# Performance work log

Measured on AMD Instinct MI355X. Metric: run time of the kernel, lower is better.

The kernel has to match this reference:

```python
import jax, jax.numpy as jnp
import numpy as np
import math

B, S, HID = 2, 1024, 2048
N_HEAD, N_KV = 16, 4
HEAD = HID // N_HEAD          # 128
N_REP = N_HEAD // N_KV        # 4


def setup_inputs() -> dict:
    key = jax.random.key(0)
    ks = jax.random.split(key, 5)
    x = jax.random.normal(ks[0], (B, S, HID), dtype=jnp.float32)
    # realistic RoPE tables: freqs over half dim, duplicated (rotate_half convention)
    inv_freq = 1.0 / (10000.0 ** (np.arange(0, HEAD, 2, dtype=np.float32) / HEAD))
    t = np.arange(S, dtype=np.float32)
    freqs = np.outer(t, inv_freq)                    # [S, HEAD/2]
    emb = np.concatenate([freqs, freqs], axis=-1)    # [S, HEAD]
    cos = jnp.asarray(np.cos(emb), dtype=jnp.float32)
    sin = jnp.asarray(np.sin(emb), dtype=jnp.float32)
    sc = 0.02
    wq = jax.random.normal(ks[1], (HID, HID), dtype=jnp.float32) * sc
    wk = jax.random.normal(ks[2], (HID, N_KV * HEAD), dtype=jnp.float32) * sc
    wv = jax.random.normal(ks[3], (HID, N_KV * HEAD), dtype=jnp.float32) * sc
    wo = jax.random.normal(ks[4], (HID, HID), dtype=jnp.float32) * sc
    return {"x": x, "cos": cos, "sin": sin, "wq": wq, "wk": wk, "wv": wv, "wo": wo}


def _rotate_half(t):
    h = t.shape[-1] // 2
    return jnp.concatenate([-t[..., h:], t[..., :h]], axis=-1)


def reference(x, cos, sin, wq, wk, wv, wo):
    b, s, _ = x.shape
    q = (x @ wq).reshape(b, s, N_HEAD, HEAD)   # [B,S,H,D]
    k = (x @ wk).reshape(b, s, N_KV, HEAD)     # [B,S,Kv,D]
    v = (x @ wv).reshape(b, s, N_KV, HEAD)
    # RoPE: cos/sin [S,D] -> [S,1,D], broadcasts over batch and heads
    c = cos[:s, None, :]
    sn = sin[:s, None, :]
    q = q * c + _rotate_half(q) * sn
    k = k * c + _rotate_half(k) * sn
    # GQA: repeat kv heads to match query heads
    k = jnp.repeat(k, N_REP, axis=2)           # [B,S,H,D]
    v = jnp.repeat(v, N_REP, axis=2)
    q = q.transpose(0, 2, 1, 3)                # [B,H,S,D]
    k = k.transpose(0, 2, 1, 3)
    v = v.transpose(0, 2, 1, 3)
    scores = jnp.einsum("bhqd,bhkd->bhqk", q, k) / math.sqrt(HEAD)
    causal = jnp.triu(jnp.full((s, s), -jnp.inf, dtype=scores.dtype), k=1)
    scores = scores + causal[None, None, :, :]
    probs = jax.nn.softmax(scores.astype(jnp.float32), axis=-1).astype(q.dtype)
    out = jnp.einsum("bhqk,bhkd->bhqd", probs, v)   # [B,H,S,D]
    out = out.transpose(0, 2, 1, 3).reshape(b, s, N_HEAD * HEAD)
    return out @ wo
```

## Files before the change

### kernel.cpp

```cpp
#include <hip/hip_runtime.h>
#include <hip/hip_bf16.h>
#include <math.h>
#include <stdint.h>

#define BATCH 2
#define SEQ   1024
#define HID   2048
#define NH    16
#define NKV   4
#define HEAD  128
#define MROWS (BATCH*SEQ)
#define QSC   0.08838834764831845f

typedef _Float16 f16;
typedef _Float16 f16x8 __attribute__((ext_vector_type(8)));
typedef __fp16   h16x2 __attribute__((ext_vector_type(2)));
typedef float    f32x4 __attribute__((ext_vector_type(4)));

__device__ __forceinline__ void glds16(const void* g, void* l) {
    __builtin_amdgcn_global_load_lds(
        (const __attribute__((address_space(1))) void*)g,
        (__attribute__((address_space(3))) void*)l, 16, 0, 0);
}

__device__ __forceinline__ f32x4 mfma16(f16x8 a, f16x8 b, f32x4 c) {
    return __builtin_amdgcn_mfma_f32_16x16x32_f16(a, b, c, 0, 0, 0);
}

__global__ __launch_bounds__(256)
void cvt_f32_f16(const float* __restrict__ in, f16* __restrict__ out) {
    int i = blockIdx.x * 256 + threadIdx.x;
    float4 v = ((const float4*)in)[i];
    union { ushort4 u; f16 h[4]; } o;
    o.h[0] = (f16)v.x; o.h[1] = (f16)v.y; o.h[2] = (f16)v.z; o.h[3] = (f16)v.w;
    ((ushort4*)out)[i] = o.u;
}

__global__ __launch_bounds__(256)
void transW(const float* __restrict__ w0, const float* __restrict__ w1,
            const float* __restrict__ w2, f16* __restrict__ out,
            int c1, int c2, int ld0, int ld1, int ld2) {
    __shared__ float t[64][65];
    const int n0 = blockIdx.x * 64, k0 = blockIdx.y * 64;
    const float* W; int ld, cb;
    if (n0 < c1)      { W = w0; ld = ld0; cb = 0;  }
    else if (n0 < c2) { W = w1; ld = ld1; cb = c1; }
    else              { W = w2; ld = ld2; cb = c2; }
    const int tr = threadIdx.x >> 4, tc = threadIdx.x & 15;
    #pragma unroll
    for (int i = 0; i < 4; ++i) {
        int row = tr * 4 + i;
        float4 v = *(const float4*)&W[(size_t)(k0 + row) * ld + (n0 - cb) + tc * 4];
        t[row][tc*4+0] = v.x; t[row][tc*4+1] = v.y;
        t[row][tc*4+2] = v.z; t[row][tc*4+3] = v.w;
    }
    __syncthreads();
    #pragma unroll
    for (int i = 0; i < 4; ++i) {
        int nrow = tr * 4 + i;
        union { ushort4 u; f16 h[4]; } o;
        o.h[0] = (f16)t[tc*4+0][nrow]; o.h[1] = (f16)t[tc*4+1][nrow];
        o.h[2] = (f16)t[tc*4+2][nrow]; o.h[3] = (f16)t[tc*4+3][nrow];
        *(ushort4*)&out[(size_t)(n0 + nrow) * 2048 + k0 + tc * 4] = o.u;
    }
}

template<int MODE>
__global__ __launch_bounds__(256, 2)
void gemm16(const f16* __restrict__ A, const f16* __restrict__ Bt,
            const float* __restrict__ cosp, const float* __restrict__ sinp,
            f16* __restrict__ Oq, f16* __restrict__ Ok, f16* __restrict__ Ov,
            float* __restrict__ Of)
{
    __shared__ f16 As[2][128 * 64];
    __shared__ f16 Bs[2][128 * 64];
    const int tid   = threadIdx.x;
    const int lane  = tid & 63;
    const int wid   = tid >> 6;
    const int col_l = lane & 15;
    const int hi    = lane >> 4;
    const int m0 = blockIdx.y * 128;
    const int n0 = blockIdx.x * 128;

    f32x4 acc[2][8];
    #pragma unroll
    for (int mt = 0; mt < 2; ++mt)
        #pragma unroll
        for (int nt = 0; nt < 8; ++nt)
            acc[mt][nt] = (f32x4){0.f, 0.f, 0.f, 0.f};

    auto stage = [&](int buf, int kt) {
        #pragma unroll
        for (int j = 0; j < 4; ++j) {
            int gidx = j * 256 + tid;
            int r = gidx >> 3, g = gidx & 7;
            int gs = (g ^ (r & 7)) << 3;
            glds16(A  + (size_t)(m0 + r) * 2048 + kt * 64 + gs,
                   (char*)&As[buf][0] + (size_t)(j * 256 + (wid << 6)) * 16);
            glds16(Bt + (size_t)(n0 + r) * 2048 + kt * 64 + gs,
                   (char*)&Bs[buf][0] + (size_t)(j * 256 + (wid << 6)) * 16);
        }
    };

    stage(0, 0);
    asm volatile("s_waitcnt vmcnt(0)" ::: "memory");
    __syncthreads();

    int cur = 0;
    #pragma unroll 1
    for (int kt = 0; kt < 32; ++kt) {
        if (kt < 31) stage(cur ^ 1, kt + 1);

        #pragma unroll
        for (int ks = 0; ks < 2; ++ks) {
            int gr = (ks << 2) | hi;
            int ar0 = wid * 32 + col_l;
            int ar1 = ar0 + 16;
            f16x8 a0 = *(const f16x8*)&As[cur][ar0 * 64 + ((gr ^ (ar0 & 7)) << 3)];
            f16x8 a1 = *(const f16x8*)&As[cur][ar1 * 64 + ((gr ^ (ar1 & 7)) << 3)];
            #pragma unroll
            for (int nt = 0; nt < 8; ++nt) {
                int br = nt * 16 + col_l;
                f16x8 b = *(const f16x8*)&Bs[cur][br * 64 + ((gr ^ (br & 7)) << 3)];
                acc[0][nt] = mfma16(a0, b, acc[0][nt]);
                acc[1][nt] = mfma16(a1, b, acc[1][nt]);
            }
        }

        if (kt < 31) {
            asm volatile("s_waitcnt vmcnt(0)" ::: "memory");
            __syncthreads();
            cur ^= 1;
        }
    }

    if (MODE == 0) {
        #pragma unroll
        for (int mt = 0; mt < 2; ++mt)
            #pragma unroll
            for (int r = 0; r < 4; ++r) {
                int grow = m0 + wid * 32 + mt * 16 + hi * 4 + r;
                #pragma unroll
                for (int nt = 0; nt < 8; ++nt)
                    Of[(size_t)grow * 2048 + n0 + nt * 16 + col_l] = acc[mt][nt][r];
            }
    } else if (n0 < 2048) {
        #pragma unroll
        for (int mt = 0; mt < 2; ++mt)
            #pragma unroll
            for (int r = 0; r < 4; ++r) {
                int grow = m0 + wid * 32 + mt * 16 + hi * 4 + r;
                int srow = grow & (SEQ - 1);
                #pragma unroll
                for (int nt = 0; nt < 4; ++nt) {
                    int d = nt * 16 + col_l;
                    float lo = acc[mt][nt][r], hv = acc[mt][nt + 4][r];
                    float cl = cosp[srow * HEAD + d],      sl = sinp[srow * HEAD + d];
                    float ch = cosp[srow * HEAD + d + 64], sh = sinp[srow * HEAD + d + 64];
                    Oq[(size_t)grow * 2048 + n0 + d]      = (f16)((lo * cl - hv * sl) * QSC);
                    Oq[(size_t)grow * 2048 + n0 + d + 64] = (f16)((hv * ch + lo * sh) * QSC);
                }
            }
    } else if (n0 < 2560) {
        #pragma unroll
        for (int mt = 0; mt < 2; ++mt)
            #pragma unroll
            for (int r = 0; r < 4; ++r) {
                int grow = m0 + wid * 32 + mt * 16 + hi * 4 + r;
                int srow = grow & (SEQ - 1);
                #pragma unroll
                for (int nt = 0; nt < 4; ++nt) {
                    int kc = (n0 - 2048) + nt * 16 + col_l;
                    int d  = kc & 127;
                    float lo = acc[mt][nt][r], hv = acc[mt][nt + 4][r];
                    float cl = cosp[srow * HEAD + d],      sl = sinp[srow * HEAD + d];
                    float ch = cosp[srow * HEAD + d + 64], sh = sinp[srow * HEAD + d + 64];
                    Ok[(size_t)grow * 512 + kc]      = (f16)(lo * cl - hv * sl);
                    Ok[(size_t)grow * 512 + kc + 64] = (f16)(hv * ch + lo * sh);
                }
            }
    } else {
        #pragma unroll
        for (int mt = 0; mt < 2; ++mt) {
            int grow0 = m0 + wid * 32 + mt * 16 + hi * 4;
            int bb = grow0 >> 10, s0 = grow0 & (SEQ - 1);
            #pragma unroll
            for (int nt = 0; nt < 8; ++nt) {
                int vcol = (n0 - 2560) + nt * 16 + col_l;
                int kvh = vcol >> 7, d = vcol & 127;
                union { ushort4 u; f16 h[4]; } pv;
                #pragma unroll
                for (int r = 0; r < 4; ++r) pv.h[r] = (f16)acc[mt][nt][r];
                *(ushort4*)&Ov[(size_t)((bb * 4 + kvh) * 128 + d) * 1024 + s0] = pv.u;
            }
        }
    }
}

__global__ __launch_bounds__(256, 2)
void attn16(const f16* __restrict__ q16, const f16* __restrict__ k16,
            const f16* __restrict__ vT, f16* __restrict__ attnb)
{
    __shared__ f16 Ks[2][32 * 128];
    __shared__ f16 Vs[2][128 * 32];

    const int tid   = threadIdx.x;
    const int lane  = tid & 63;
    const int wid   = tid >> 6;
    const int col_l = lane & 15;
    const int hi    = lane >> 4;

    const int bx = blockIdx.x;
    const int qt = (bx < 256) ? (15 - (bx >> 5)) : ((bx - 256) >> 5);
    const int bh = bx & 31;
    const int b  = bh >> 4;
    const int h  = bh & 15;
    const int kv = h >> 2;
    const int qrow = qt * 64 + wid * 16 + col_l;

    f16x8 qf[4];
    {
        const f16* qp = q16 + (size_t)(b * SEQ + qrow) * 2048 + h * 128 + hi * 8;
        #pragma unroll
        for (int ks = 0; ks < 4; ++ks) qf[ks] = *(const f16x8*)&qp[ks * 32];
    }
    const f16* vTg = vT + (size_t)(b * 4 + kv) * 128 * 1024;

    auto stage = [&](int buf, int kt) {
        #pragma unroll
        for (int j = 0; j < 2; ++j) {
            int gidx = j * 256 + tid;
            int r = gidx >> 4, g = gidx & 15;
            glds16(k16 + (size_t)(b * SEQ + kt * 32 + r) * 512 + kv * 128 + ((g ^ (r & 7)) << 3),
                   (char*)&Ks[buf][0] + (size_t)(j * 256 + (wid << 6)) * 16);
            int d = gidx >> 2, g2 = gidx & 3;
            glds16(vTg + (size_t)d * 1024 + kt * 32 + ((g2 ^ (d & 3)) << 3),
                   (char*)&Vs[buf][0] + (size_t)(j * 256 + (wid << 6)) * 16);
        }
    };

    f32x4 O[8];
    #pragma unroll
    for (int dt = 0; dt < 8; ++dt) O[dt] = (f32x4){0.f, 0.f, 0.f, 0.f};
    float mrun = -INFINITY, lrun = 0.f;

    const int ntiles = 2 * (qt + 1);
    stage(0, 0);
    asm volatile("s_waitcnt vmcnt(0)" ::: "memory");
    __syncthreads();

    int cur = 0;
    #pragma unroll 1
    for (int kt = 0; kt < ntiles; ++kt) {
        if (kt + 1 < ntiles) stage(cur ^ 1, kt + 1);

        f32x4 S0 = (f32x4){0.f,0.f,0.f,0.f}, S1 = (f32x4){0.f,0.f,0.f,0.f};
        #pragma unroll
        for (int ks = 0; ks < 4; ++ks) {
            int gr = (ks << 2) | hi;
            int r0 = col_l, r1 = col_l + 16;
            f16x8 kf0 = *(const f16x8*)&Ks[cur][r0 * 128 + ((gr ^ (r0 & 7)) << 3)];
            f16x8 kf1 = *(const f16x8*)&Ks[cur][r1 * 128 + ((gr ^ (r1 & 7)) << 3)];
            S0 = mfma16(kf0, qf[ks], S0);
            S1 = mfma16(kf1, qf[ks], S1);
        }
        float p[8];
        p[0]=S0[0]; p[1]=S0[1]; p[2]=S0[2]; p[3]=S0[3];
        p[4]=S1[0]; p[5]=S1[1]; p[6]=S1[2]; p[7]=S1[3];

        #pragma unroll
        for (int sl = 0; sl < 8; ++sl) {
            int kk = kt * 32 + (sl >> 2) * 16 + hi * 4 + (sl & 3);
            if (kk > qrow) p[sl] = -INFINITY;
        }

        float mt = p[0];
        #pragma unroll
        for (int sl = 1; sl < 8; ++sl) mt = fmaxf(mt, p[sl]);
        mt = fmaxf(mt, __shfl_xor(mt, 16));
        mt = fmaxf(mt, __shfl_xor(mt, 32));
        float mnew = fmaxf(mrun, mt);
        float corr = __expf(mrun - mnew);
        mrun = mnew;
        float ps = 0.f;
        #pragma unroll
        for (int sl = 0; sl < 8; ++sl) { p[sl] = __expf(p[sl] - mnew); ps += p[sl]; }
        ps += __shfl_xor(ps, 16);
        ps += __shfl_xor(ps, 32);
        lrun = lrun * corr + ps;

        union U2 { h16x2 h; int i; };
        int pk[4];
        { U2 u; u.h = __builtin_amdgcn_cvt_pkrtz(p[0], p[1]); pk[0] = u.i; }
        { U2 u; u.h = __builtin_amdgcn_cvt_pkrtz(p[2], p[3]); pk[1] = u.i; }
        { U2 u; u.h = __builtin_amdgcn_cvt_pkrtz(p[4], p[5]); pk[2] = u.i; }
        { U2 u; u.h = __builtin_amdgcn_cvt_pkrtz(p[6], p[7]); pk[3] = u.i; }
        union UA { f16x8 v; int i[4]; } ua;
        #pragma unroll
        for (int j = 0; j < 4; ++j) {
            int srcl = col_l + 16 * ((2 * hi + (j >> 1)) & 3);
            int v0 = __builtin_amdgcn_ds_bpermute(srcl << 2, pk[j & 1]);
            int v1 = __builtin_amdgcn_ds_bpermute(srcl << 2, pk[(j & 1) + 2]);
            ua.i[j] = (hi >= 2) ? v1 : v0;
        }

        float cb[4];
        #pragma unroll
        for (int r = 0; r < 4; ++r)
            cb[r] = __int_as_float(__builtin_amdgcn_ds_bpermute((hi * 4 + r) << 2,
                                                                __float_as_int(corr)));
        #pragma unroll
        for (int dt = 0; dt < 8; ++dt) {
            O[dt][0] *= cb[0]; O[dt][1] *= cb[1];
            O[dt][2] *= cb[2]; O[dt][3] *= cb[3];
        }

        #pragma unroll
        for (int dt = 0; dt < 8; ++dt) {
            int vr = dt * 16 + col_l;
            f16x8 vf = *(const f16x8*)&Vs[cur][vr * 32 + (((hi) ^ (vr & 3)) << 3)];
            O[dt] = mfma16(ua.v, vf, O[dt]);
        }

        if (kt + 1 < ntiles) {
            asm volatile("s_waitcnt vmcnt(0)" ::: "memory");
            __syncthreads();
            cur ^= 1;
        }
    }

    float linv = 1.f / lrun;
    float lb[4];
    #pragma unroll
    for (int r = 0; r < 4; ++r)
        lb[r] = __int_as_float(__builtin_amdgcn_ds_bpermute((hi * 4 + r) << 2,
                                                            __float_as_int(linv)));
    #pragma unroll
    for (int dt = 0; dt < 8; ++dt)
        #pragma unroll
        for (int r = 0; r < 4; ++r) {
            int row = b * SEQ + qt * 64 + wid * 16 + hi * 4 + r;
            attnb[(size_t)row * 2048 + h * 128 + dt * 16 + col_l] = (f16)(O[dt][r] * lb[r]);
        }
}

extern "C" void kernel_launch(void* const* d_in, const int* in_sizes, int n_in,
                              void* d_out, int out_size, void* d_ws, size_t ws_size,
                              hipStream_t stream)
{
    const float* x    = (const float*)d_in[0];
    const float* cosp = (const float*)d_in[1];
    const float* sinp = (const float*)d_in[2];
    const float* wq   = (const float*)d_in[3];
    const float* wk   = (const float*)d_in[4];
    const float* wv   = (const float*)d_in[5];
    const float* wo   = (const float*)d_in[6];
    float* out = (float*)d_out;

    char* ws = (char*)d_ws;
    f16* x16    = (f16*)(ws);
    f16* attn16v= (f16*)(ws);
    f16* Wqkvt  = (f16*)(ws + 8388608);
    f16* Wot    = (f16*)(ws + 8388608);
    f16* q16    = (f16*)(ws + 20971520);
    f16* k16    = (f16*)(ws + 29360128);
    f16* vT     = (f16*)(ws + 31457280);

    cvt_f32_f16<<<4096, 256, 0, stream>>>(x, x16);

    transW<<<dim3(48, 32), 256, 0, stream>>>(wq, wk, wv, Wqkvt, 2048, 2560, 2048, 512, 512);

    gemm16<1><<<dim3(24, 16), 256, 0, stream>>>(x16, Wqkvt, cosp, sinp,
                                                q16, k16, vT, nullptr);

    transW<<<dim3(32, 32), 256, 0, stream>>>(wo, wo, wo, Wot, 2048, 2048, 2048, 2048, 2048);

    attn16<<<dim3(512), 256, 0, stream>>>(q16, k16, vT, attn16v);

    gemm16<0><<<dim3(16, 16), 256, 0, stream>>>(attn16v, Wot, nullptr, nullptr,
                                                nullptr, nullptr, nullptr, out);
}
```

Baseline: 227.5 us.

## Shrink GEMM N-tile to 64, add XCD swizzle, move RoPE to separate kernel

The GEMM tile shrinks from 128x128 to 128x64, which doubles the grid to 768 and 512 blocks so the GPU's compute units are better filled. Block IDs are remapped across the 8 XCDs, and LDS double buffering is dropped for a single buffer with load-then-compute per k-step. The RoPE rotation and Q scaling move out of the GEMM epilogue, which can no longer see both halves of a head, into a separate elementwise kernel. This costs an extra read-write pass over Q and K, an extra f16 rounding before the rotation, and loses the overlap of loads with compute.

```diff
diff --git a/kernel.cpp b/kernel.cpp
--- a/kernel.cpp
+++ b/kernel.cpp
@@ -66,72 +66,70 @@
 }
 
 template<int MODE>
-__global__ __launch_bounds__(256, 2)
+__global__ __launch_bounds__(256)
 void gemm16(const f16* __restrict__ A, const f16* __restrict__ Bt,
-            const float* __restrict__ cosp, const float* __restrict__ sinp,
             f16* __restrict__ Oq, f16* __restrict__ Ok, f16* __restrict__ Ov,
-            float* __restrict__ Of)
+            float* __restrict__ Of, int ntn)
 {
-    __shared__ f16 As[2][128 * 64];
-    __shared__ f16 Bs[2][128 * 64];
+    __shared__ f16 As[128 * 64];
+    __shared__ f16 Bs[64 * 64];
     const int tid   = threadIdx.x;
     const int lane  = tid & 63;
     const int wid   = tid >> 6;
     const int col_l = lane & 15;
     const int hi    = lane >> 4;
-    const int m0 = blockIdx.y * 128;
-    const int n0 = blockIdx.x * 128;
-
-    f32x4 acc[2][8];
+
+    const int nwg = gridDim.x;
+    const int cpx = nwg >> 3;
+    const int bid = blockIdx.x;
+    const int sw  = (bid & 7) * cpx + (bid >> 3);
+    const int n0  = (sw % ntn) * 64;
+    const int m0  = (sw / ntn) * 128;
+
+    f32x4 acc[2][4];
     #pragma unroll
     for (int mt = 0; mt < 2; ++mt)
         #pragma unroll
-        for (int nt = 0; nt < 8; ++nt)
+        for (int nt = 0; nt < 4; ++nt)
             acc[mt][nt] = (f32x4){0.f, 0.f, 0.f, 0.f};
 
-    auto stage = [&](int buf, int kt) {
+    #pragma unroll 1
+    for (int kt = 0; kt < 32; ++kt) {
         #pragma unroll
         for (int j = 0; j < 4; ++j) {
             int gidx = j * 256 + tid;
             int r = gidx >> 3, g = gidx & 7;
             int gs = (g ^ (r & 7)) << 3;
-            glds16(A  + (size_t)(m0 + r) * 2048 + kt * 64 + gs,
-                   (char*)&As[buf][0] + (size_t)(j * 256 + (wid << 6)) * 16);
+            glds16(A + (size_t)(m0 + r) * 2048 + kt * 64 + gs,
+                   (char*)As + (size_t)(j * 256 + (wid << 6)) * 16);
+        }
+        #pragma unroll
+        for (int j = 0; j < 2; ++j) {
+            int gidx = j * 256 + tid;
+            int r = gidx >> 3, g = gidx & 7;
+            int gs = (g ^ (r & 7)) << 3;
             glds16(Bt + (size_t)(n0 + r) * 2048 + kt * 64 + gs,
-                   (char*)&Bs[buf][0] + (size_t)(j * 256 + (wid << 6)) * 16);
-        }
-    };
-
-    stage(0, 0);
-    asm volatile("s_waitcnt vmcnt(0)" ::: "memory");
-    __syncthreads();
-
-    int cur = 0;
-    #pragma unroll 1
-    for (int kt = 0; kt < 32; ++kt) {
-        if (kt < 31) stage(cur ^ 1, kt + 1);
+                   (char*)Bs + (size_t)(j * 256 + (wid << 6)) * 16);
+        }
+        asm volatile("s_waitcnt vmcnt(0)" ::: "memory");
+        __syncthreads();
 
         #pragma unroll
         for (int ks = 0; ks < 2; ++ks) {
             int gr = (ks << 2) | hi;
             int ar0 = wid * 32 + col_l;
             int ar1 = ar0 + 16;
-            f16x8 a0 = *(const f16x8*)&As[cur][ar0 * 64 + ((gr ^ (ar0 & 7)) << 3)];
-            f16x8 a1 = *(const f16x8*)&As[cur][ar1 * 64 + ((gr ^ (ar1 & 7)) << 3)];
+            f16x8 a0 = *(const f16x8*)&As[ar0 * 64 + ((gr ^ (ar0 & 7)) << 3)];
+            f16x8 a1 = *(const f16x8*)&As[ar1 * 64 + ((gr ^ (ar1 & 7)) << 3)];
             #pragma unroll
-            for (int nt = 0; nt < 8; ++nt) {
+            for (int nt = 0; nt < 4; ++nt) {
                 int br = nt * 16 + col_l;
-                f16x8 b = *(const f16x8*)&Bs[cur][br * 64 + ((gr ^ (br & 7)) << 3)];
+                f16x8 b = *(const f16x8*)&Bs[br * 64 + ((gr ^ (br & 7)) << 3)];
                 acc[0][nt] = mfma16(a0, b, acc[0][nt]);
                 acc[1][nt] = mfma16(a1, b, acc[1][nt]);
             }
         }
-
-        if (kt < 31) {
-            asm volatile("s_waitcnt vmcnt(0)" ::: "memory");
-            __syncthreads();
-            cur ^= 1;
-        }
+        __syncthreads();
     }
 
     if (MODE == 0) {
@@ -141,7 +139,7 @@
             for (int r = 0; r < 4; ++r) {
                 int grow = m0 + wid * 32 + mt * 16 + hi * 4 + r;
                 #pragma unroll
-                for (int nt = 0; nt < 8; ++nt)
+                for (int nt = 0; nt < 4; ++nt)
                     Of[(size_t)grow * 2048 + n0 + nt * 16 + col_l] = acc[mt][nt][r];
             }
     } else if (n0 < 2048) {
@@ -150,16 +148,9 @@
             #pragma unroll
             for (int r = 0; r < 4; ++r) {
                 int grow = m0 + wid * 32 + mt * 16 + hi * 4 + r;
-                int srow = grow & (SEQ - 1);
                 #pragma unroll
-                for (int nt = 0; nt < 4; ++nt) {
-                    int d = nt * 16 + col_l;
-                    float lo = acc[mt][nt][r], hv = acc[mt][nt + 4][r];
-                    float cl = cosp[srow * HEAD + d],      sl = sinp[srow * HEAD + d];
-                    float ch = cosp[srow * HEAD + d + 64], sh = sinp[srow * HEAD + d + 64];
-                    Oq[(size_t)grow * 2048 + n0 + d]      = (f16)((lo * cl - hv * sl) * QSC);
-                    Oq[(size_t)grow * 2048 + n0 + d + 64] = (f16)((hv * ch + lo * sh) * QSC);
-                }
+                for (int nt = 0; nt < 4; ++nt)
+                    Oq[(size_t)grow * 2048 + n0 + nt * 16 + col_l] = (f16)acc[mt][nt][r];
             }
     } else if (n0 < 2560) {
         #pragma unroll
@@ -167,17 +158,9 @@
             #pragma unroll
             for (int r = 0; r < 4; ++r) {
                 int grow = m0 + wid * 32 + mt * 16 + hi * 4 + r;
-                int srow = grow & (SEQ - 1);
                 #pragma unroll
-                for (int nt = 0; nt < 4; ++nt) {
-                    int kc = (n0 - 2048) + nt * 16 + col_l;
-                    int d  = kc & 127;
-                    float lo = acc[mt][nt][r], hv = acc[mt][nt + 4][r];
-                    float cl = cosp[srow * HEAD + d],      sl = sinp[srow * HEAD + d];
-                    float ch = cosp[srow * HEAD + d + 64], sh = sinp[srow * HEAD + d + 64];
-                    Ok[(size_t)grow * 512 + kc]      = (f16)(lo * cl - hv * sl);
-                    Ok[(size_t)grow * 512 + kc + 64] = (f16)(hv * ch + lo * sh);
-                }
+                for (int nt = 0; nt < 4; ++nt)
+                    Ok[(size_t)grow * 512 + (n0 - 2048) + nt * 16 + col_l] = (f16)acc[mt][nt][r];
             }
     } else {
         #pragma unroll
@@ -185,7 +168,7 @@
             int grow0 = m0 + wid * 32 + mt * 16 + hi * 4;
             int bb = grow0 >> 10, s0 = grow0 & (SEQ - 1);
             #pragma unroll
-            for (int nt = 0; nt < 8; ++nt) {
+            for (int nt = 0; nt < 4; ++nt) {
                 int vcol = (n0 - 2560) + nt * 16 + col_l;
                 int kvh = vcol >> 7, d = vcol & 127;
                 union { ushort4 u; f16 h[4]; } pv;
@@ -195,6 +178,41 @@
             }
         }
     }
+}
+
+__global__ __launch_bounds__(256)
+void rope_qk(f16* __restrict__ q16, f16* __restrict__ k16,
+             const float* __restrict__ cosp, const float* __restrict__ sinp)
+{
+    int t = blockIdx.x * 256 + threadIdx.x;
+    f16* p; int row, head, quad; float sc;
+    if (t < 2048 * 256) {
+        row = t >> 8; int rem = t & 255; head = rem >> 4; quad = rem & 15;
+        p = q16 + (size_t)row * 2048 + head * 128 + quad * 4;
+        sc = QSC;
+    } else {
+        int u = t - 2048 * 256;
+        row = u >> 6; int rem = u & 63; head = rem >> 4; quad = rem & 15;
+        p = k16 + (size_t)row * 512 + head * 128 + quad * 4;
+        sc = 1.f;
+    }
+    const int srow = row & (SEQ - 1);
+    const int d0 = quad * 4;
+    float4 c4 = *(const float4*)&cosp[srow * HEAD + d0];
+    float4 s4 = *(const float4*)&sinp[srow * HEAD + d0];
+    union { ushort4 u; f16 h[4]; } lo, hv, olo, ohi;
+    lo.u = *(ushort4*)p;
+    hv.u = *(ushort4*)(p + 64);
+    const float c[4] = {c4.x, c4.y, c4.z, c4.w};
+    const float s[4] = {s4.x, s4.y, s4.z, s4.w};
+    #pragma unroll
+    for (int e = 0; e < 4; ++e) {
+        float fl = (float)lo.h[e], fh = (float)hv.h[e];
+        olo.h[e] = (f16)((fl * c[e] - fh * s[e]) * sc);
+        ohi.h[e] = (f16)((fh * c[e] + fl * s[e]) * sc);
+    }
+    *(ushort4*)p        = olo.u;
+    *(ushort4*)(p + 64) = ohi.u;
 }
 
 __global__ __launch_bounds__(256, 2)
@@ -370,13 +388,13 @@
 
     transW<<<dim3(48, 32), 256, 0, stream>>>(wq, wk, wv, Wqkvt, 2048, 2560, 2048, 512, 512);
 
-    gemm16<1><<<dim3(24, 16), 256, 0, stream>>>(x16, Wqkvt, cosp, sinp,
-                                                q16, k16, vT, nullptr);
+    gemm16<1><<<768, 256, 0, stream>>>(x16, Wqkvt, q16, k16, vT, nullptr, 48);
+
+    rope_qk<<<2560, 256, 0, stream>>>(q16, k16, cosp, sinp);
 
     transW<<<dim3(32, 32), 256, 0, stream>>>(wo, wo, wo, Wot, 2048, 2048, 2048, 2048, 2048);
 
-    attn16<<<dim3(512), 256, 0, stream>>>(q16, k16, vT, attn16v);
-
-    gemm16<0><<<dim3(16, 16), 256, 0, stream>>>(attn16v, Wot, nullptr, nullptr,
-                                                nullptr, nullptr, nullptr, out);
-}
+    attn16<<<512, 256, 0, stream>>>(q16, k16, vT, attn16v);
+
+    gemm16<0><<<512, 256, 0, stream>>>(attn16v, Wot, nullptr, nullptr, nullptr, out, 32);
+}
```

Measured after the change: 220.6 us. 1.03x faster.
